# Kernel tuning notes

Measured on AMD Instinct MI355X. Metric: run time of the kernel, lower is better.

## Reference

```python
import jax, jax.numpy as jnp
import numpy as np

N, DIM, HID, E = 100000, 128, 512, 600000


def setup_inputs() -> dict:
    key = jax.random.key(0)
    k_h, k_src, k_dst, k_w1, k_b1, k_w2, k_b2 = jax.random.split(key, 7)
    h = jax.random.normal(k_h, (N, DIM), dtype=jnp.float32)
    src = jax.random.randint(k_src, (E,), 0, N)
    dst = jax.random.randint(k_dst, (E,), 0, N)
    edge_index = jnp.stack([src, dst], axis=0).astype(jnp.int64)
    # Linear params stored as [in, out] (math-equivalent to torch's [out,in].T)
    s1 = 1.0 / np.sqrt(2 * DIM)
    s2 = 1.0 / np.sqrt(HID)
    W1 = jax.random.uniform(k_w1, (2 * DIM, HID), jnp.float32, -s1, s1)
    b1 = jax.random.uniform(k_b1, (HID,), jnp.float32, -s1, s1)
    W2 = jax.random.uniform(k_w2, (HID, DIM), jnp.float32, -s2, s2)
    b2 = jax.random.uniform(k_b2, (DIM,), jnp.float32, -s2, s2)
    return {"h": h, "edge_index": edge_index, "W1": W1, "b1": b1, "W2": W2, "b2": b2}


def reference(h, edge_index, W1, b1, W2, b2):
    src, dst = edge_index[0], edge_index[1]
    n = h.shape[0]
    # scatter-mean: sum gathered neighbor features per destination node
    agg_sum = jax.ops.segment_sum(h[src], dst, num_segments=n)  # [N, DIM]
    deg = jax.ops.segment_sum(jnp.ones((src.shape[0],), h.dtype), dst, num_segments=n)  # [N]
    mean = agg_sum / jnp.maximum(deg, 1.0)[:, None]
    # isolated nodes (deg==0) fall back to their own features
    agg = jnp.where((deg == 0)[:, None], h, mean)
    x = jnp.concatenate([h, agg], axis=-1)  # [N, 2*DIM]
    hdn = jax.nn.gelu(x @ W1 + b1, approximate=False)  # torch GELU default = exact erf
    return hdn @ W2 + b2
```

## Files before the change

### kernel.cpp

```cpp
#include <hip/hip_runtime.h>
#include <hip/hip_bf16.h>
#include <math.h>

#define N_NODES 100000
#define DIM 128
#define HID 512
#define EDGES 600000
#define SCAN_CHUNK 1024
#define SCAN_NBLK ((N_NODES + SCAN_CHUNK - 1) / SCAN_CHUNK)
#define MROWS_PAD 100096

typedef short bf16x8 __attribute__((ext_vector_type(8)));
typedef float f32x4 __attribute__((ext_vector_type(4)));


__device__ inline unsigned short f32_to_bf16(float f) {
    unsigned int u = __float_as_uint(f);
    u += 0x7fff + ((u >> 16) & 1);
    return (unsigned short)(u >> 16);
}

__device__ inline float gelu_f(float x) {
    float x3 = x * x * x;
    float y = 0.7978845608028654f * x + 0.0356774081f * x3;
    float e = exp2f(y * 2.8853900817779268f);
    float t = 1.0f - 2.0f * __builtin_amdgcn_rcpf(e + 1.0f);
    return 0.5f * x * (1.0f + t);
}

__device__ inline void gload16(const void* g, void* l) {
    __builtin_amdgcn_global_load_lds(
        (const __attribute__((address_space(1))) unsigned int*)g,
        (__attribute__((address_space(3))) unsigned int*)l,
        16, 0, 0);
}

#define PREP_W1_BLKS 512
#define PREP_W2_BLKS 128
#define PREP_CONV_BLKS 12500
#define PREP_COUNT_BLKS ((EDGES + 255) / 256)
#define PREP_TOTAL (PREP_W1_BLKS + PREP_W2_BLKS + PREP_CONV_BLKS + PREP_COUNT_BLKS)

__global__ __launch_bounds__(256) void mgl_prep_kernel(
    const float* __restrict__ h, const int* __restrict__ ei,
    const float* __restrict__ W1, const float* __restrict__ W2,
    unsigned short* __restrict__ X, unsigned short* __restrict__ W1T,
    unsigned short* __restrict__ W2T, int* __restrict__ cnt)
{
    int b = blockIdx.x;
    if (b < PREP_W1_BLKS) {
        int n = b;
        int k = threadIdx.x;
        unsigned short val = f32_to_bf16(W1[(size_t)k * HID + n]);
        int byteoff = (k * 2) ^ ((n & 7) << 4);
        *(unsigned short*)((char*)(W1T + (size_t)n * 256) + byteoff) = val;
        return;
    }
    b -= PREP_W1_BLKS;
    if (b < PREP_W2_BLKS) {
        int n = b;
        #pragma unroll
        for (int it = 0; it < 2; ++it) {
            int k = threadIdx.x + it * 256;
            unsigned short val = f32_to_bf16(W2[(size_t)k * DIM + n]);
            int byteoff = (k * 2) ^ ((n & 7) << 4);
            *(unsigned short*)((char*)(W2T + (size_t)n * 512) + byteoff) = val;
        }
        return;
    }
    b -= PREP_W2_BLKS;
    if (b < PREP_CONV_BLKS) {
        int t = b * 256 + threadIdx.x;
        if (t >= N_NODES * (DIM / 4)) return;
        int node = t >> 5;
        int c4 = t & 31;
        float4 v = *(const float4*)(h + (size_t)node * DIM + c4 * 4);
        ushort4 p;
        p.x = f32_to_bf16(v.x); p.y = f32_to_bf16(v.y);
        p.z = f32_to_bf16(v.z); p.w = f32_to_bf16(v.w);
        int byteoff = (c4 * 8) ^ ((node & 7) << 4);
        *(ushort4*)((char*)(X + (size_t)node * 256) + byteoff) = p;
        return;
    }
    b -= PREP_CONV_BLKS;
    {
        int e = b * 256 + threadIdx.x;
        if (e < EDGES) atomicAdd(&cnt[ei[EDGES + e]], 1);
    }
}

__global__ __launch_bounds__(256) void mgl_scan_block_kernel(
    const int* __restrict__ cnt, int* __restrict__ row_start, int* __restrict__ bsum)
{
    __shared__ int sdata[256];
    int t = threadIdx.x;
    int base = blockIdx.x * SCAN_CHUNK + t * 4;
    int v[4];
    #pragma unroll
    for (int i = 0; i < 4; ++i) {
        int idx = base + i;
        v[i] = (idx < N_NODES) ? cnt[idx] : 0;
    }
    int tsum = v[0] + v[1] + v[2] + v[3];
    sdata[t] = tsum;
    __syncthreads();
    for (int off = 1; off < 256; off <<= 1) {
        int x = (t >= off) ? sdata[t - off] : 0;
        __syncthreads();
        sdata[t] += x;
        __syncthreads();
    }
    int run = (t > 0) ? sdata[t - 1] : 0;
    #pragma unroll
    for (int i = 0; i < 4; ++i) {
        int idx = base + i;
        if (idx < N_NODES) row_start[idx] = run;
        run += v[i];
    }
    if (t == 255) bsum[blockIdx.x] = sdata[255];
}

__global__ __launch_bounds__(128) void mgl_scan_bsum_kernel(int* __restrict__ bsum)
{
    __shared__ int sd[128];
    int t = threadIdx.x;
    int v = (t < SCAN_NBLK) ? bsum[t] : 0;
    sd[t] = v;
    __syncthreads();
    for (int off = 1; off < 128; off <<= 1) {
        int x = (t >= off) ? sd[t - off] : 0;
        __syncthreads();
        sd[t] += x;
        __syncthreads();
    }
    if (t < SCAN_NBLK) bsum[t] = sd[t] - v;
}

__global__ __launch_bounds__(256) void mgl_scan_add_kernel(
    int* __restrict__ row_start, const int* __restrict__ bsum)
{
    int i = blockIdx.x * 256 + threadIdx.x;
    if (i < N_NODES) row_start[i] += bsum[i / SCAN_CHUNK];
    if (i == 0) row_start[N_NODES] = EDGES;
}

__global__ __launch_bounds__(256) void mgl_fill_kernel(
    const int* __restrict__ ei, const int* __restrict__ row_start,
    int* __restrict__ cnt, int* __restrict__ csr)
{
    int e = blockIdx.x * 256 + threadIdx.x;
    if (e >= EDGES) return;
    int s = ei[e];
    int t = ei[EDGES + e];
    int pos = atomicSub(&cnt[t], 1) - 1;
    csr[row_start[t] + pos] = s;
}

__global__ __launch_bounds__(256) void mgl_gather_mean_kernel(
    const unsigned short* __restrict__ Xb, const int* __restrict__ row_start,
    const int* __restrict__ csr, unsigned short* __restrict__ X)
{
    int v = blockIdx.x * 4 + (threadIdx.x >> 6);
    if (v >= N_NODES) return;
    int lane = threadIdx.x & 63;
    int beg = row_start[v];
    int nb = row_start[v + 1] - beg;
    int laneByte = lane * 4;
    const char* xb = (const char*)Xb;

    if (nb > 0) {
        float2 acc = make_float2(0.f, 0.f);
        for (int base = 0; base < nb; base += 64) {
            int rem = nb - base; if (rem > 64) rem = 64;
            int sv = (lane < rem) ? csr[beg + base + lane] : 0;
            for (int j = 0; j < rem; ++j) {
                int s = __shfl(sv, j);
                unsigned int pk = *(const unsigned int*)(
                    xb + (size_t)s * 512 + (laneByte ^ ((s & 7) << 4)));
                acc.x += __uint_as_float(pk << 16);
                acc.y += __uint_as_float(pk & 0xffff0000u);
            }
        }
        float inv = 1.f / (float)nb;
        unsigned int po = (unsigned int)f32_to_bf16(acc.x * inv) |
                          ((unsigned int)f32_to_bf16(acc.y * inv) << 16);
        *(unsigned int*)((char*)(X + (size_t)v * 256) +
                         ((256 + laneByte) ^ ((v & 7) << 4))) = po;
    } else {
        unsigned int pk = *(const unsigned int*)(
            xb + (size_t)v * 512 + (laneByte ^ ((v & 7) << 4)));
        *(unsigned int*)((char*)(X + (size_t)v * 256) +
                         ((256 + laneByte) ^ ((v & 7) << 4))) = pk;
    }
}

template<int KTOT, int NY, bool GELU_OUT>
__global__ __launch_bounds__(512) void mgl_gemm_kernel(
    const unsigned short* __restrict__ Wt,
    const unsigned short* __restrict__ Xr,
    const float* __restrict__ bias,
    void* __restrict__ outp)
{
    constexpr int NT = KTOT / 64;
    __shared__ unsigned short ldsW[128 * 64];
    __shared__ unsigned short ldsX[256 * 64];

    int tid = threadIdx.x;
    int w = tid >> 6;
    int l = tid & 63;

    int bid = blockIdx.x;
    if (NY > 1) {
        int nwg = gridDim.x;
        int q = nwg >> 3, r = nwg & 7;
        int xcd = bid & 7, idx = bid >> 3;
        bid = (xcd < r ? xcd * (q + 1) : r * (q + 1) + (xcd - r) * q) + idx;
    }
    int m0 = (bid / NY) * 256;
    int n0 = (bid % NY) * 128;

    int wm = w >> 1;
    int wn = w & 1;
    int r16 = l & 15;
    int kq = l >> 4;
    int rowmask = (r16 & 7) << 4;

    f32x4 acc[4][4] = {};

    int srow = tid >> 3;
    int scol = (tid & 7) << 4;

    for (int kt = 0; kt < NT; ++kt) {
        #pragma unroll
        for (int i = 0; i < 2; ++i) {
            int row = i * 64 + srow;
            const char* g = (const char*)Wt +
                (size_t)(n0 + row) * (KTOT * 2) + kt * 128 + scol;
            gload16(g, (char*)ldsW + i * 8192 + tid * 16);
        }
        #pragma unroll
        for (int i = 0; i < 4; ++i) {
            int gm = m0 + i * 64 + srow;
            if (gm > N_NODES - 1) gm = N_NODES - 1;
            const char* g = (const char*)Xr +
                (size_t)gm * (KTOT * 2) + kt * 128 + scol;
            gload16(g, (char*)ldsX + i * 8192 + tid * 16);
        }
        __syncthreads();

        #pragma unroll
        for (int kk = 0; kk < 2; ++kk) {
            int posb = (kk * 64 + kq * 16) ^ rowmask;
            bf16x8 a[4], b[4];
            #pragma unroll
            for (int ni = 0; ni < 4; ++ni)
                a[ni] = *(const bf16x8*)((const char*)ldsW +
                          (wn * 64 + ni * 16 + r16) * 128 + posb);
            #pragma unroll
            for (int mi = 0; mi < 4; ++mi)
                b[mi] = *(const bf16x8*)((const char*)ldsX +
                          (wm * 64 + mi * 16 + r16) * 128 + posb);
            #pragma unroll
            for (int mi = 0; mi < 4; ++mi)
                #pragma unroll
                for (int ni = 0; ni < 4; ++ni)
                    acc[mi][ni] = __builtin_amdgcn_mfma_f32_16x16x32_bf16(
                        a[ni], b[mi], acc[mi][ni], 0, 0, 0);
        }
        __syncthreads();
    }

    #pragma unroll
    for (int mi = 0; mi < 4; ++mi) {
        int m = m0 + wm * 64 + mi * 16 + r16;
        if (m >= N_NODES) continue;
        #pragma unroll
        for (int ni = 0; ni < 4; ++ni) {
            int nc = n0 + wn * 64 + ni * 16 + kq * 4;
            float4 bv = *(const float4*)(bias + nc);
            float x0 = acc[mi][ni][0] + bv.x;
            float x1 = acc[mi][ni][1] + bv.y;
            float x2 = acc[mi][ni][2] + bv.z;
            float x3 = acc[mi][ni][3] + bv.w;
            if (GELU_OUT) {
                ushort4 p;
                p.x = f32_to_bf16(gelu_f(x0));
                p.y = f32_to_bf16(gelu_f(x1));
                p.z = f32_to_bf16(gelu_f(x2));
                p.w = f32_to_bf16(gelu_f(x3));
                unsigned short* row = (unsigned short*)outp + (size_t)m * HID;
                int byteoff = (nc * 2) ^ ((m & 7) << 4);
                *(ushort4*)((char*)row + byteoff) = p;
            } else {
                float4 o = make_float4(x0, x1, x2, x3);
                *(float4*)((float*)outp + (size_t)m * DIM + nc) = o;
            }
        }
    }
}

extern "C" void kernel_launch(void* const* d_in, const int* in_sizes, int n_in,
                              void* d_out, int out_size, void* d_ws, size_t ws_size,
                              hipStream_t stream) {
    const float* h  = (const float*)d_in[0];
    const int*   ei = (const int*)d_in[1];
    const float* W1 = (const float*)d_in[2];
    const float* b1 = (const float*)d_in[3];
    const float* W2 = (const float*)d_in[4];
    const float* b2 = (const float*)d_in[5];
    float* out = (float*)d_out;

    unsigned short* X   = (unsigned short*)d_ws;
    unsigned short* hdn = X + (size_t)MROWS_PAD * 256;
    unsigned short* W1T = hdn + (size_t)MROWS_PAD * 512;
    unsigned short* W2T = W1T + 512 * 256;
    int* cnt = (int*)(W2T + 128 * 512);
    int* row_start = cnt + N_NODES;
    int* bsum = row_start + N_NODES + 1;
    int* csr = bsum + 128;

    hipMemsetAsync(cnt, 0, N_NODES * sizeof(int), stream);
    mgl_prep_kernel<<<PREP_TOTAL, 256, 0, stream>>>(h, ei, W1, W2, X, W1T, W2T, cnt);
    mgl_scan_block_kernel<<<SCAN_NBLK, 256, 0, stream>>>(cnt, row_start, bsum);
    mgl_scan_bsum_kernel<<<1, 128, 0, stream>>>(bsum);
    mgl_scan_add_kernel<<<(N_NODES + 255) / 256, 256, 0, stream>>>(row_start, bsum);
    mgl_fill_kernel<<<(EDGES + 255) / 256, 256, 0, stream>>>(ei, row_start, cnt, csr);
    mgl_gather_mean_kernel<<<(N_NODES + 3) / 4, 256, 0, stream>>>(X, row_start, csr, X);

    int mtiles = MROWS_PAD / 256;
    mgl_gemm_kernel<256, 4, true><<<mtiles * 4, 512, 0, stream>>>(W1T, X, b1, hdn);
    mgl_gemm_kernel<512, 1, false><<<mtiles, 512, 0, stream>>>(W2T, hdn, b2, out);
}
```

Before: 221.7 us.

## Make MLP GEMMs persistent with resident weights and double-buffered X loads

Replaces the two one-tile-per-block GEMM launches with persistent 256-block kernels. Each block keeps its whole weight slice in LDS and walks over several 256-row M tiles. X tiles are double-buffered, so the next k-chunk is prefetched while MFMAs run, and waits are expressed with explicit vmcnt and barrier calls. Weight reloads and per-tile launch overhead go away, at the cost of about 128KB of LDS per block (one block per CU) and hand-managed synchronisation. The second GEMM now uses a narrower 64-column N slice per block, so the N dimension is split across blocks where it was not before.

```diff
diff --git a/kernel.cpp b/kernel.cpp
--- a/kernel.cpp
+++ b/kernel.cpp
@@ -194,106 +194,126 @@
     }
 }
 
-template<int KTOT, int NY, bool GELU_OUT>
-__global__ __launch_bounds__(512) void mgl_gemm_kernel(
+template<int KTOT, int NI, int NGROUPS, int PARTS, bool GELU_OUT>
+__global__ __launch_bounds__(512) void mgl_mlp_kernel(
     const unsigned short* __restrict__ Wt,
     const unsigned short* __restrict__ Xr,
     const float* __restrict__ bias,
     void* __restrict__ outp)
 {
     constexpr int NT = KTOT / 64;
-    __shared__ unsigned short ldsW[128 * 64];
-    __shared__ unsigned short ldsX[256 * 64];
+    constexpr int KB = KTOT * 2;
+    constexpr int WROWS = NI * 32;
+    constexpr int SHIFT = (NT == 4) ? 2 : 3;
+    constexpr int TILES = MROWS_PAD / 256;
+
+    __shared__ char lds[65536 + 2 * 32768];
+    char* ldsW = lds;
+    char* ldsX = lds + 65536;
 
     int tid = threadIdx.x;
-    int w = tid >> 6;
-    int l = tid & 63;
-
-    int bid = blockIdx.x;
-    if (NY > 1) {
-        int nwg = gridDim.x;
-        int q = nwg >> 3, r = nwg & 7;
-        int xcd = bid & 7, idx = bid >> 3;
-        bid = (xcd < r ? xcd * (q + 1) : r * (q + 1) + (xcd - r) * q) + idx;
-    }
-    int m0 = (bid / NY) * 256;
-    int n0 = (bid % NY) * 128;
-
-    int wm = w >> 1;
-    int wn = w & 1;
-    int r16 = l & 15;
-    int kq = l >> 4;
+    int w = tid >> 6, l = tid & 63;
+
+    int vbid = ((blockIdx.x & 7) << 5) + (blockIdx.x >> 3);
+    int p = vbid / NGROUPS;
+    int ng = vbid % NGROUPS;
+    int T = (TILES - p + PARTS - 1) / PARTS;
+    int C = T << SHIFT;
+
+    int wm = w >> 1, wn = w & 1;
+    int r16 = l & 15, kq = l >> 4;
     int rowmask = (r16 & 7) << 4;
 
-    f32x4 acc[4][4] = {};
-
-    int srow = tid >> 3;
-    int scol = (tid & 7) << 4;
-
-    for (int kt = 0; kt < NT; ++kt) {
+    {
+        const char* wg = (const char*)Wt + (size_t)ng * WROWS * KB;
         #pragma unroll
-        for (int i = 0; i < 2; ++i) {
-            int row = i * 64 + srow;
-            const char* g = (const char*)Wt +
-                (size_t)(n0 + row) * (KTOT * 2) + kt * 128 + scol;
-            gload16(g, (char*)ldsW + i * 8192 + tid * 16);
-        }
+        for (int i = 0; i < 8; ++i) {
+            int byte = i * 8192 + tid * 16;
+            int row = byte / KB, col = byte & (KB - 1);
+            gload16(wg + (size_t)row * KB + col, ldsW + byte);
+        }
+    }
+    {
+        int m0 = p * 256;
         #pragma unroll
         for (int i = 0; i < 4; ++i) {
-            int gm = m0 + i * 64 + srow;
-            if (gm > N_NODES - 1) gm = N_NODES - 1;
-            const char* g = (const char*)Xr +
-                (size_t)gm * (KTOT * 2) + kt * 128 + scol;
-            gload16(g, (char*)ldsX + i * 8192 + tid * 16);
-        }
-        __syncthreads();
+            int byte = i * 8192 + tid * 16;
+            int row = byte >> 7, col = byte & 127;
+            gload16((const char*)Xr + (size_t)(m0 + row) * KB + col, ldsX + byte);
+        }
+    }
+
+    f32x4 acc[4][NI] = {};
+
+    for (int c = 0; c < C; ++c) {
+        int kt = c & (NT - 1);
+        char* bufc = ldsX + (c & 1) * 32768;
+        if (c + 1 < C) {
+            int c2 = c + 1;
+            int kt2 = c2 & (NT - 1);
+            int m02 = (p + (c2 >> SHIFT) * PARTS) * 256;
+            char* bufn = ldsX + (c2 & 1) * 32768;
+            #pragma unroll
+            for (int i = 0; i < 4; ++i) {
+                int byte = i * 8192 + tid * 16;
+                int row = byte >> 7, col = byte & 127;
+                gload16((const char*)Xr + (size_t)(m02 + row) * KB + kt2 * 128 + col,
+                        bufn + byte);
+            }
+            asm volatile("s_waitcnt vmcnt(4)" ::: "memory");
+        } else {
+            asm volatile("s_waitcnt vmcnt(0)" ::: "memory");
+        }
+        __builtin_amdgcn_s_barrier();
 
         #pragma unroll
         for (int kk = 0; kk < 2; ++kk) {
             int posb = (kk * 64 + kq * 16) ^ rowmask;
-            bf16x8 a[4], b[4];
-            #pragma unroll
-            for (int ni = 0; ni < 4; ++ni)
-                a[ni] = *(const bf16x8*)((const char*)ldsW +
-                          (wn * 64 + ni * 16 + r16) * 128 + posb);
+            bf16x8 a[NI], b[4];
+            #pragma unroll
+            for (int ni = 0; ni < NI; ++ni)
+                a[ni] = *(const bf16x8*)(ldsW +
+                    (size_t)(wn * (NI * 16) + ni * 16 + r16) * KB + kt * 128 + posb);
             #pragma unroll
             for (int mi = 0; mi < 4; ++mi)
-                b[mi] = *(const bf16x8*)((const char*)ldsX +
-                          (wm * 64 + mi * 16 + r16) * 128 + posb);
+                b[mi] = *(const bf16x8*)(bufc + (wm * 64 + mi * 16 + r16) * 128 + posb);
             #pragma unroll
             for (int mi = 0; mi < 4; ++mi)
                 #pragma unroll
-                for (int ni = 0; ni < 4; ++ni)
+                for (int ni = 0; ni < NI; ++ni)
                     acc[mi][ni] = __builtin_amdgcn_mfma_f32_16x16x32_bf16(
                         a[ni], b[mi], acc[mi][ni], 0, 0, 0);
         }
-        __syncthreads();
-    }
-
-    #pragma unroll
-    for (int mi = 0; mi < 4; ++mi) {
-        int m = m0 + wm * 64 + mi * 16 + r16;
-        if (m >= N_NODES) continue;
-        #pragma unroll
-        for (int ni = 0; ni < 4; ++ni) {
-            int nc = n0 + wn * 64 + ni * 16 + kq * 4;
-            float4 bv = *(const float4*)(bias + nc);
-            float x0 = acc[mi][ni][0] + bv.x;
-            float x1 = acc[mi][ni][1] + bv.y;
-            float x2 = acc[mi][ni][2] + bv.z;
-            float x3 = acc[mi][ni][3] + bv.w;
-            if (GELU_OUT) {
-                ushort4 p;
-                p.x = f32_to_bf16(gelu_f(x0));
-                p.y = f32_to_bf16(gelu_f(x1));
-                p.z = f32_to_bf16(gelu_f(x2));
-                p.w = f32_to_bf16(gelu_f(x3));
-                unsigned short* row = (unsigned short*)outp + (size_t)m * HID;
-                int byteoff = (nc * 2) ^ ((m & 7) << 4);
-                *(ushort4*)((char*)row + byteoff) = p;
-            } else {
-                float4 o = make_float4(x0, x1, x2, x3);
-                *(float4*)((float*)outp + (size_t)m * DIM + nc) = o;
+        __builtin_amdgcn_s_barrier();
+
+        if (kt == NT - 1) {
+            int m0 = (p + (c >> SHIFT) * PARTS) * 256;
+            #pragma unroll
+            for (int mi = 0; mi < 4; ++mi) {
+                int m = m0 + wm * 64 + mi * 16 + r16;
+                #pragma unroll
+                for (int ni = 0; ni < NI; ++ni) {
+                    int nc = ng * (NI * 32) + wn * (NI * 16) + ni * 16 + kq * 4;
+                    float4 bv = *(const float4*)(bias + nc);
+                    float x0 = acc[mi][ni][0] + bv.x;
+                    float x1 = acc[mi][ni][1] + bv.y;
+                    float x2 = acc[mi][ni][2] + bv.z;
+                    float x3 = acc[mi][ni][3] + bv.w;
+                    if (GELU_OUT) {
+                        ushort4 pk;
+                        pk.x = f32_to_bf16(gelu_f(x0));
+                        pk.y = f32_to_bf16(gelu_f(x1));
+                        pk.z = f32_to_bf16(gelu_f(x2));
+                        pk.w = f32_to_bf16(gelu_f(x3));
+                        unsigned short* row = (unsigned short*)outp + (size_t)m * HID;
+                        int byteoff = (nc * 2) ^ ((m & 7) << 4);
+                        *(ushort4*)((char*)row + byteoff) = pk;
+                    } else if (m < N_NODES) {
+                        float4 o = make_float4(x0, x1, x2, x3);
+                        *(float4*)((float*)outp + (size_t)m * DIM + nc) = o;
+                    }
+                    acc[mi][ni] = (f32x4){0.f, 0.f, 0.f, 0.f};
+                }
             }
         }
     }
@@ -327,7 +347,6 @@
     mgl_fill_kernel<<<(EDGES + 255) / 256, 256, 0, stream>>>(ei, row_start, cnt, csr);
     mgl_gather_mean_kernel<<<(N_NODES + 3) / 4, 256, 0, stream>>>(X, row_start, csr, X);
 
-    int mtiles = MROWS_PAD / 256;
-    mgl_gemm_kernel<256, 4, true><<<mtiles * 4, 512, 0, stream>>>(W1T, X, b1, hdn);
-    mgl_gemm_kernel<512, 1, false><<<mtiles, 512, 0, stream>>>(W2T, hdn, b2, out);
-}
+    mgl_mlp_kernel<256, 4, 4, 64, true><<<256, 512, 0, stream>>>(W1T, X, b1, hdn);
+    mgl_mlp_kernel<512, 2, 2, 128, false><<<256, 512, 0, stream>>>(W2T, hdn, b2, out);
+}
```

Result: slower. 233.3 us (+5.2%).

## Fuse both MLP GEMMs into one kernel keeping hidden activations on-chip

Applied to the files above, without the earlier changes.

Replaces the two separate GEMM launches with a single fused kernel. Each 128-row block holds its X rows in registers, computes the hidden layer 64 columns at a time, applies GELU, stages the result in per-wave LDS, and accumulates the second GEMM directly. This removes the global write and reread of the 100k x 512 bf16 hidden tensor and one kernel launch. In exchange, each block now streams all of W1 and W2 through LDS, there is a sync per hidden chunk, and the per-wave MFMA tiles are smaller, which may lower tensor-core efficiency.

```diff
diff --git a/kernel.cpp b/kernel.cpp
--- a/kernel.cpp
+++ b/kernel.cpp
@@ -194,107 +194,100 @@
     }
 }
 
-template<int KTOT, int NY, bool GELU_OUT>
-__global__ __launch_bounds__(512) void mgl_gemm_kernel(
-    const unsigned short* __restrict__ Wt,
+__global__ __launch_bounds__(512, 4) void mgl_fused_mlp_kernel(
+    const unsigned short* __restrict__ W1T,
+    const unsigned short* __restrict__ W2T,
     const unsigned short* __restrict__ Xr,
-    const float* __restrict__ bias,
-    void* __restrict__ outp)
-{
-    constexpr int NT = KTOT / 64;
-    __shared__ unsigned short ldsW[128 * 64];
-    __shared__ unsigned short ldsX[256 * 64];
-
-    int tid = threadIdx.x;
-    int w = tid >> 6;
-    int l = tid & 63;
-
-    int bid = blockIdx.x;
-    if (NY > 1) {
-        int nwg = gridDim.x;
-        int q = nwg >> 3, r = nwg & 7;
-        int xcd = bid & 7, idx = bid >> 3;
-        bid = (xcd < r ? xcd * (q + 1) : r * (q + 1) + (xcd - r) * q) + idx;
-    }
-    int m0 = (bid / NY) * 256;
-    int n0 = (bid % NY) * 128;
-
-    int wm = w >> 1;
-    int wn = w & 1;
-    int r16 = l & 15;
-    int kq = l >> 4;
-    int rowmask = (r16 & 7) << 4;
-
-    f32x4 acc[4][4] = {};
-
-    int srow = tid >> 3;
-    int scol = (tid & 7) << 4;
-
-    for (int kt = 0; kt < NT; ++kt) {
-        #pragma unroll
-        for (int i = 0; i < 2; ++i) {
-            int row = i * 64 + srow;
-            const char* g = (const char*)Wt +
-                (size_t)(n0 + row) * (KTOT * 2) + kt * 128 + scol;
-            gload16(g, (char*)ldsW + i * 8192 + tid * 16);
-        }
-        #pragma unroll
-        for (int i = 0; i < 4; ++i) {
-            int gm = m0 + i * 64 + srow;
-            if (gm > N_NODES - 1) gm = N_NODES - 1;
-            const char* g = (const char*)Xr +
-                (size_t)gm * (KTOT * 2) + kt * 128 + scol;
-            gload16(g, (char*)ldsX + i * 8192 + tid * 16);
-        }
-        __syncthreads();
-
-        #pragma unroll
-        for (int kk = 0; kk < 2; ++kk) {
-            int posb = (kk * 64 + kq * 16) ^ rowmask;
-            bf16x8 a[4], b[4];
+    const float* __restrict__ b1f, const float* __restrict__ b2f,
+    float* __restrict__ outp)
+{
+    __shared__ char lds[65536];
+    char* W1l = lds;
+    char* W2l = lds + 32768;
+    const int tid = threadIdx.x;
+    const int w = tid >> 6, l = tid & 63;
+    const int r16 = l & 15, kq = l >> 4;
+    const int rmask = (r16 & 7) << 4;
+    char* bnc = lds + 49152 + w * 2048;
+
+    const size_t m0 = (size_t)blockIdx.x * 128;
+    const size_t m = m0 + w * 16 + r16;
+
+    bf16x8 xf[8];
+    {
+        const char* xrow = (const char*)Xr + m * 512;
+        int swz = ((int)m & 7) << 4;
+        #pragma unroll
+        for (int ks = 0; ks < 8; ++ks)
+            xf[ks] = *(const bf16x8*)(xrow + ((ks * 64 + kq * 16) ^ swz));
+    }
+
+    f32x4 acc[8] = {};
+
+    for (int t = 0; t < 8; ++t) {
+        {
+            const char* src = (const char*)W1T + (size_t)t * 32768;
             #pragma unroll
-            for (int ni = 0; ni < 4; ++ni)
-                a[ni] = *(const bf16x8*)((const char*)ldsW +
-                          (wn * 64 + ni * 16 + r16) * 128 + posb);
+            for (int i = 0; i < 4; ++i) {
+                int off = i * 8192 + tid * 16;
+                gload16(src + off, W1l + off);
+            }
+        }
+        {
             #pragma unroll
-            for (int mi = 0; mi < 4; ++mi)
-                b[mi] = *(const bf16x8*)((const char*)ldsX +
-                          (wm * 64 + mi * 16 + r16) * 128 + posb);
+            for (int i = 0; i < 2; ++i) {
+                int p = tid + i * 512;
+                int o = p >> 3, c16 = (p & 7) * 16;
+                const char* src = (const char*)W2T + (size_t)o * 1024 + t * 128 + c16;
+                gload16(src, W2l + o * 128 + c16);
+            }
+        }
+        __syncthreads();
+
+        #pragma unroll
+        for (int ni = 0; ni < 4; ++ni) {
+            f32x4 s = {};
             #pragma unroll
-            for (int mi = 0; mi < 4; ++mi)
-                #pragma unroll
-                for (int ni = 0; ni < 4; ++ni)
-                    acc[mi][ni] = __builtin_amdgcn_mfma_f32_16x16x32_bf16(
-                        a[ni], b[mi], acc[mi][ni], 0, 0, 0);
-        }
-        __syncthreads();
-    }
-
-    #pragma unroll
-    for (int mi = 0; mi < 4; ++mi) {
-        int m = m0 + wm * 64 + mi * 16 + r16;
-        if (m >= N_NODES) continue;
-        #pragma unroll
-        for (int ni = 0; ni < 4; ++ni) {
-            int nc = n0 + wn * 64 + ni * 16 + kq * 4;
-            float4 bv = *(const float4*)(bias + nc);
-            float x0 = acc[mi][ni][0] + bv.x;
-            float x1 = acc[mi][ni][1] + bv.y;
-            float x2 = acc[mi][ni][2] + bv.z;
-            float x3 = acc[mi][ni][3] + bv.w;
-            if (GELU_OUT) {
-                ushort4 p;
-                p.x = f32_to_bf16(gelu_f(x0));
-                p.y = f32_to_bf16(gelu_f(x1));
-                p.z = f32_to_bf16(gelu_f(x2));
-                p.w = f32_to_bf16(gelu_f(x3));
-                unsigned short* row = (unsigned short*)outp + (size_t)m * HID;
-                int byteoff = (nc * 2) ^ ((m & 7) << 4);
-                *(ushort4*)((char*)row + byteoff) = p;
-            } else {
-                float4 o = make_float4(x0, x1, x2, x3);
-                *(float4*)((float*)outp + (size_t)m * DIM + nc) = o;
-            }
+            for (int ks = 0; ks < 8; ++ks) {
+                bf16x8 a = *(const bf16x8*)(W1l + (ni * 16 + r16) * 512 +
+                                            ((ks * 64 + kq * 16) ^ rmask));
+                s = __builtin_amdgcn_mfma_f32_16x16x32_bf16(a, xf[ks], s, 0, 0, 0);
+            }
+            float4 bv = *(const float4*)(b1f + t * 64 + ni * 16 + kq * 4);
+            float g0 = gelu_f(s[0] + bv.x);
+            float g1 = gelu_f(s[1] + bv.y);
+            float g2 = gelu_f(s[2] + bv.z);
+            float g3 = gelu_f(s[3] + bv.w);
+            uint2 pk;
+            pk.x = (unsigned int)f32_to_bf16(g0) | ((unsigned int)f32_to_bf16(g1) << 16);
+            pk.y = (unsigned int)f32_to_bf16(g2) | ((unsigned int)f32_to_bf16(g3) << 16);
+            *(uint2*)(bnc + r16 * 128 + ((ni * 32 + kq * 8) ^ rmask)) = pk;
+        }
+
+        #pragma unroll
+        for (int c = 0; c < 2; ++c) {
+            bf16x8 b = *(const bf16x8*)(bnc + r16 * 128 + ((c * 64 + kq * 16) ^ rmask));
+            #pragma unroll
+            for (int oi = 0; oi < 8; ++oi) {
+                bf16x8 a = *(const bf16x8*)(W2l + (oi * 16 + r16) * 128 +
+                                            ((c * 64 + kq * 16) ^ rmask));
+                acc[oi] = __builtin_amdgcn_mfma_f32_16x16x32_bf16(a, b, acc[oi], 0, 0, 0);
+            }
+        }
+        __syncthreads();
+    }
+
+    if (m < N_NODES) {
+        float* orow = outp + m * DIM;
+        #pragma unroll
+        for (int oi = 0; oi < 8; ++oi) {
+            float4 bv = *(const float4*)(b2f + oi * 16 + kq * 4);
+            float4 o;
+            o.x = acc[oi][0] + bv.x;
+            o.y = acc[oi][1] + bv.y;
+            o.z = acc[oi][2] + bv.z;
+            o.w = acc[oi][3] + bv.w;
+            *(float4*)(orow + oi * 16 + kq * 4) = o;
         }
     }
 }
@@ -311,8 +304,7 @@
     float* out = (float*)d_out;
 
     unsigned short* X   = (unsigned short*)d_ws;
-    unsigned short* hdn = X + (size_t)MROWS_PAD * 256;
-    unsigned short* W1T = hdn + (size_t)MROWS_PAD * 512;
+    unsigned short* W1T = X + (size_t)MROWS_PAD * 256;
     unsigned short* W2T = W1T + 512 * 256;
     int* cnt = (int*)(W2T + 128 * 512);
     int* row_start = cnt + N_NODES;
@@ -327,7 +319,6 @@
     mgl_fill_kernel<<<(EDGES + 255) / 256, 256, 0, stream>>>(ei, row_start, cnt, csr);
     mgl_gather_mean_kernel<<<(N_NODES + 3) / 4, 256, 0, stream>>>(X, row_start, csr, X);
 
-    int mtiles = MROWS_PAD / 256;
-    mgl_gemm_kernel<256, 4, true><<<mtiles * 4, 512, 0, stream>>>(W1T, X, b1, hdn);
-    mgl_gemm_kernel<512, 1, false><<<mtiles, 512, 0, stream>>>(W2T, hdn, b2, out);
-}
+    mgl_fused_mlp_kernel<<<MROWS_PAD / 128, 512, 0, stream>>>(
+        W1T, W2T, X, b1, b2, out);
+}
```

Result: slower. 234.4 us (+5.7%).
